# Kernel optimization log

Measured on AMD Instinct MI355X. Metric: run time of the kernel, lower is better.

## Reference

```python
import jax, jax.numpy as jnp
import numpy as np
from jax import lax

B, T, E, D, A, C, FILT = 32, 1600, 1024, 1024, 512, 10, 100
SCALING = 2.0


def setup_inputs() -> dict:
    key = jax.random.key(0)
    ks = jax.random.split(key, 14)
    enc_hs_pad = jax.random.normal(ks[0], (B, T, E), dtype=jnp.float32)
    # lengths in [T//2, T] so every row has valid positions
    enc_hs_len = jax.random.randint(ks[1], (B,), T // 2, T + 1, dtype=jnp.int32)
    dec_z = jax.random.normal(ks[2], (B, D), dtype=jnp.float32)
    # previous attention weights: uniform over valid frames, normalized
    valid = (jnp.arange(T)[None, :] < enc_hs_len[:, None]).astype(jnp.float32)
    raw = jax.random.uniform(ks[3], (B, T), dtype=jnp.float32) * valid
    att_prev = raw / jnp.sum(raw, axis=1, keepdims=True)
    att_h = 0.1 * jax.random.normal(ks[4], (B, A), dtype=jnp.float32)
    att_c = 0.1 * jax.random.normal(ks[5], (B, A), dtype=jnp.float32)
    W_enc = jax.random.normal(ks[6], (A, E), dtype=jnp.float32) / np.sqrt(E)
    b_enc = jax.random.normal(ks[7], (A,), dtype=jnp.float32) * 0.01
    W_dec = jax.random.normal(ks[8], (A, D), dtype=jnp.float32) / np.sqrt(D)
    conv_w = jax.random.normal(ks[9], (C, 1, 2 * FILT + 1), dtype=jnp.float32) / np.sqrt(2 * FILT + 1)
    W_ih = jax.random.normal(ks[10], (4 * A, C), dtype=jnp.float32) / np.sqrt(C)
    W_hh = jax.random.normal(ks[11], (4 * A, A), dtype=jnp.float32) / np.sqrt(A)
    W_g = jax.random.normal(ks[12], (A,), dtype=jnp.float32) / np.sqrt(A)
    b_g = jnp.zeros((1,), dtype=jnp.float32)
    return {"enc_hs_pad": enc_hs_pad, "enc_hs_len": enc_hs_len, "dec_z": dec_z,
            "att_prev": att_prev, "att_h": att_h, "att_c": att_c,
            "W_enc": W_enc, "b_enc": b_enc, "W_dec": W_dec, "conv_w": conv_w,
            "W_ih": W_ih, "W_hh": W_hh, "W_g": W_g, "b_g": b_g}


def reference(enc_hs_pad, enc_hs_len, dec_z, att_prev, att_h, att_c,
              W_enc, b_enc, W_dec, conv_w, W_ih, W_hh, W_g, b_g):
    t_len = enc_hs_pad.shape[1]
    filts = (conv_w.shape[-1] - 1) // 2

    # precompute encoder projection (B, T, A)
    pre_enc = jnp.einsum('bte,ae->bta', enc_hs_pad, W_enc) + b_enc

    # location conv on previous attention: (B,1,T) -> (B,C,T), relu, global max-pool over T
    att_conv = lax.conv_general_dilated(att_prev[:, None, :], conv_w,
                                        window_strides=(1,), padding=[(filts, filts)],
                                        dimension_numbers=('NCH', 'OIH', 'NCH'))
    att_feat = jnp.max(jax.nn.relu(att_conv), axis=-1)  # (B, C)

    # LSTMCell (no bias), pytorch gate order i, f, g, o
    gates = att_feat @ W_ih.T + att_h @ W_hh.T  # (B, 4A)
    i, f, g, o = jnp.split(gates, 4, axis=-1)
    c_new = jax.nn.sigmoid(f) * att_c + jax.nn.sigmoid(i) * jnp.tanh(g)
    h_new = jax.nn.sigmoid(o) * jnp.tanh(c_new)  # (B, A)

    dec_proj = dec_z @ W_dec.T  # (B, A)
    # scores (B, T)
    e = jnp.tanh(h_new[:, None, :] + pre_enc + dec_proj[:, None, :]) @ W_g + b_g

    mask = jnp.arange(t_len)[None, :] >= enc_hs_len[:, None]  # True = pad
    e = jnp.where(mask, jnp.finfo(e.dtype).min, e)
    w = jax.nn.softmax(SCALING * e, axis=1)  # (B, T)

    ctx = jnp.einsum('bt,bte->be', w, enc_hs_pad)  # (B, E)
    return ctx, w, h_new, c_new
```

## Files before the change

kernel.cpp:

```cpp
#include <hip/hip_runtime.h>
#include <hip/hip_bf16.h>

#define BB 32
#define TT 1600
#define EE 1024
#define AA 512
#define CC 10
#define KW 201

typedef __attribute__((ext_vector_type(8))) short short8;
typedef __attribute__((ext_vector_type(4))) float f32x4;

__device__ __forceinline__ float sigm(float x) { return 1.f / (1.f + expf(-x)); }

__device__ __forceinline__ unsigned int cvt2(float a, float b) {
    float2 f2; f2.x = a; f2.y = b;
    __hip_bfloat162 h = __float22bfloat162_rn(f2);
    unsigned int r;
    __builtin_memcpy(&r, &h, 4);
    return r;
}

__device__ __forceinline__ void gl_lds16(const void* g, void* l) {
    __builtin_amdgcn_global_load_lds(
        (const __attribute__((address_space(1))) unsigned int*)g,
        (__attribute__((address_space(3))) unsigned int*)l, 16, 0, 0);
}

#define AF_OFF   0
#define R_OFF    320
#define E_OFF    16704
#define WBF_OFF  67904

#define CTX_OFF 0
#define W_OFF   32768
#define H_OFF   83968
#define C_OFF   100352

__global__ void prep_kernel(const float* __restrict__ att_prev,
                            const float* __restrict__ conv_w,
                            const float* __restrict__ W_enc,
                            float* __restrict__ af,
                            unsigned short* __restrict__ Wbf) {
    int bx = blockIdx.x, tid = threadIdx.x;
    if (bx >= 320) {
        int i = (bx - 320) * 256 + tid;
        float4 v = reinterpret_cast<const float4*>(W_enc)[i];
        uint2 p;
        p.x = cvt2(v.x, v.y);
        p.y = cvt2(v.z, v.w);
        reinterpret_cast<uint2*>(Wbf)[i] = p;
        return;
    }
    int b = bx / 10, c = bx % 10;
    __shared__ float xs[1808];
    __shared__ float wsm[KW];
    __shared__ float red[256];
    const float* xp = att_prev + b * TT;
    for (int i = tid; i < 1808; i += 256) {
        int g = i - 100;
        xs[i] = (g >= 0 && g < TT) ? xp[g] : 0.f;
    }
    if (tid < KW) wsm[tid] = conv_w[c * KW + tid];
    __syncthreads();
    float mx = 0.f;
    #pragma unroll 1
    for (int sweep = 0; sweep < 2; ++sweep) {
        int t0 = sweep * 1024 + tid * 4;
        if (t0 >= TT) break;
        float a0 = xs[t0], a1 = xs[t0 + 1], a2 = xs[t0 + 2], a3 = xs[t0 + 3];
        float s0 = 0.f, s1 = 0.f, s2 = 0.f, s3 = 0.f;
        #pragma unroll 4
        for (int k = 0; k < KW; ++k) {
            float w = wsm[k];
            s0 += w * a0; s1 += w * a1; s2 += w * a2; s3 += w * a3;
            a0 = a1; a1 = a2; a2 = a3;
            a3 = xs[t0 + k + 4];
        }
        mx = fmaxf(mx, fmaxf(fmaxf(s0, s1), fmaxf(s2, s3)));
    }
    red[tid] = mx; __syncthreads();
    for (int s = 128; s > 0; s >>= 1) {
        if (tid < s) red[tid] = fmaxf(red[tid], red[tid + s]);
        __syncthreads();
    }
    if (tid == 0) af[b * CC + c] = red[0];
}

__global__ void gates_lstm_kernel(const float* __restrict__ af,
                                  const float* __restrict__ att_h,
                                  const float* __restrict__ dec_z,
                                  const float* __restrict__ att_c,
                                  const float* __restrict__ W_ih,
                                  const float* __restrict__ W_hh,
                                  const float* __restrict__ W_dec,
                                  float* __restrict__ out,
                                  float* __restrict__ r_ws) {
    __shared__ float gsm[8][32];
    __shared__ float dsm[8][32];
    int tid = threadIdx.x;
    int a0 = blockIdx.x * 2;
    int b = tid & 31;
    if (tid < 256) {
        int u = tid >> 5;
        int gate = u >> 1, ai = u & 1;
        int j = gate * 512 + a0 + ai;
        float s = 0.f;
        #pragma unroll
        for (int k = 0; k < 10; ++k) s += af[b * 10 + k] * W_ih[j * 10 + k];
        const float4* wr = reinterpret_cast<const float4*>(W_hh + (size_t)j * 512);
        const float4* hr = reinterpret_cast<const float4*>(att_h + b * 512);
        #pragma unroll 4
        for (int k = 0; k < 128; ++k) {
            float4 w = wr[k], h = hr[k];
            s += w.x * h.x + w.y * h.y + w.z * h.z + w.w * h.w;
        }
        gsm[u][b] = s;
    } else {
        int v = (tid - 256) >> 5;
        int ai = v & 1, q = v >> 1;
        int a = a0 + ai;
        const float4* wr = reinterpret_cast<const float4*>(W_dec + (size_t)a * 1024) + q * 64;
        const float4* zr = reinterpret_cast<const float4*>(dec_z + (size_t)b * 1024) + q * 64;
        float s = 0.f;
        #pragma unroll 4
        for (int k = 0; k < 64; ++k) {
            float4 w = wr[k], z = zr[k];
            s += w.x * z.x + w.y * z.y + w.z * z.z + w.w * z.w;
        }
        dsm[v][b] = s;
    }
    __syncthreads();
    if (tid < 64) {
        int ai = tid >> 5;
        int a = a0 + ai;
        float ig = gsm[ai][b], fg = gsm[2 + ai][b], gg = gsm[4 + ai][b], og = gsm[6 + ai][b];
        float cn = sigm(fg) * att_c[b * 512 + a] + sigm(ig) * tanhf(gg);
        float hn = sigm(og) * tanhf(cn);
        out[H_OFF + b * 512 + a] = hn;
        out[C_OFF + b * 512 + a] = cn;
        float dec = dsm[ai][b] + dsm[2 + ai][b] + dsm[4 + ai][b] + dsm[6 + ai][b];
        r_ws[b * 512 + a] = hn + dec;
    }
}

__global__ void __launch_bounds__(1024, 4)
score_gemm_kernel(const float* __restrict__ enc,
                  const unsigned short* __restrict__ Wbf,
                  const float* __restrict__ b_enc,
                  const float* __restrict__ r_ws,
                  const float* __restrict__ W_g,
                  float* __restrict__ e_ws) {
    __shared__ __align__(16) short As[2][4096];
    __shared__ __align__(16) short Bs[2][8192];
    __shared__ float e_part[8][128];

    int tid = threadIdx.x;
    int lane = tid & 63, wv = tid >> 6;
    int wm = wv >> 3, wn = wv & 7;
    int col = lane & 15, quad = lane >> 4;
    int m0 = blockIdx.x * 128;

    const unsigned short* bsrc = Wbf + (size_t)((tid >> 6) * 16 + (tid & 15)) * EE
                                 + ((tid >> 4) & 3) * 8;
    int arow = tid >> 3, akq2 = tid & 7;
    const float* asrc = enc + (size_t)(m0 + arow) * EE + akq2 * 4;
    int adst = (arow >> 4) * 512 + ((akq2 >> 1) * 16 + (arow & 15)) * 8 + (akq2 & 1) * 4;

    f32x4 acc[4][2][2];
    #pragma unroll
    for (int mt = 0; mt < 4; ++mt)
        #pragma unroll
        for (int h = 0; h < 2; ++h)
            #pragma unroll
            for (int nt = 0; nt < 2; ++nt)
                acc[mt][h][nt] = (f32x4){0.f, 0.f, 0.f, 0.f};

    {
        gl_lds16(bsrc, &Bs[0][tid * 8]);
        float4 v = *reinterpret_cast<const float4*>(asrc);
        uint2 p; p.x = cvt2(v.x, v.y); p.y = cvt2(v.z, v.w);
        *reinterpret_cast<uint2*>(&As[0][adst]) = p;
    }
    __syncthreads();

    int bufA = 0;
    for (int k0 = 0; k0 < EE; k0 += 32) {
        bool last = (k0 == EE - 32);
        gl_lds16(bsrc + (size_t)256 * EE + k0, &Bs[1][tid * 8]);
        short8 a_frag[4];
        #pragma unroll
        for (int mt = 0; mt < 4; ++mt)
            a_frag[mt] = *reinterpret_cast<const short8*>(
                &As[bufA][(wm * 4 + mt) * 512 + (quad * 16 + col) * 8]);
        #pragma unroll
        for (int nt = 0; nt < 2; ++nt) {
            short8 bf = *reinterpret_cast<const short8*>(
                &Bs[0][(wn * 2 + nt) * 512 + (quad * 16 + col) * 8]);
            #pragma unroll
            for (int mt = 0; mt < 4; ++mt)
                acc[mt][0][nt] = __builtin_amdgcn_mfma_f32_16x16x32_bf16(
                    a_frag[mt], bf, acc[mt][0][nt], 0, 0, 0);
        }
        __syncthreads();
        float4 av;
        if (!last) {
            av = *reinterpret_cast<const float4*>(asrc + k0 + 32);
            gl_lds16(bsrc + k0 + 32, &Bs[0][tid * 8]);
        }
        #pragma unroll
        for (int nt = 0; nt < 2; ++nt) {
            short8 bf = *reinterpret_cast<const short8*>(
                &Bs[1][(wn * 2 + nt) * 512 + (quad * 16 + col) * 8]);
            #pragma unroll
            for (int mt = 0; mt < 4; ++mt)
                acc[mt][1][nt] = __builtin_amdgcn_mfma_f32_16x16x32_bf16(
                    a_frag[mt], bf, acc[mt][1][nt], 0, 0, 0);
        }
        if (!last) {
            uint2 p; p.x = cvt2(av.x, av.y); p.y = cvt2(av.z, av.w);
            *reinterpret_cast<uint2*>(&As[bufA ^ 1][adst]) = p;
        }
        __syncthreads();
        bufA ^= 1;
    }

    float wg[2][2], bn[2][2];
    #pragma unroll
    for (int h = 0; h < 2; ++h)
        #pragma unroll
        for (int nt = 0; nt < 2; ++nt) {
            int n = h * 256 + wn * 32 + nt * 16 + col;
            wg[h][nt] = W_g[n];
            bn[h][nt] = b_enc[n];
        }
    #pragma unroll
    for (int mt = 0; mt < 4; ++mt) {
        int mg = m0 + wm * 64 + mt * 16;
        int bb = mg / TT;
        float rr[2][2];
        #pragma unroll
        for (int h = 0; h < 2; ++h)
            #pragma unroll
            for (int nt = 0; nt < 2; ++nt)
                rr[h][nt] = r_ws[bb * AA + h * 256 + wn * 32 + nt * 16 + col];
        #pragma unroll
        for (int reg = 0; reg < 4; ++reg) {
            float p = 0.f;
            #pragma unroll
            for (int h = 0; h < 2; ++h)
                #pragma unroll
                for (int nt = 0; nt < 2; ++nt)
                    p += wg[h][nt] * tanhf(acc[mt][h][nt][reg] + bn[h][nt] + rr[h][nt]);
            p += __shfl_xor(p, 1);
            p += __shfl_xor(p, 2);
            p += __shfl_xor(p, 4);
            p += __shfl_xor(p, 8);
            if (col == 0) e_part[wn][wm * 64 + mt * 16 + quad * 4 + reg] = p;
        }
    }
    __syncthreads();
    if (tid < 128) {
        float s = 0.f;
        #pragma unroll
        for (int i = 0; i < 8; ++i) s += e_part[i][tid];
        e_ws[m0 + tid] = s;
    }
}

__global__ void ctx_softmax_kernel(const float* __restrict__ enc,
                                   const float* __restrict__ e_ws,
                                   const int* __restrict__ lens,
                                   float* __restrict__ w_out,
                                   float* __restrict__ ctx) {
    int b = blockIdx.x, ch = blockIdx.y;
    int tid = threadIdx.x;
    __shared__ float w_sm[1600];
    __shared__ float red[512];
    __shared__ float part[8][128];
    int len = lens[b];
    const float* e = e_ws + b * TT;
    float mx = -3.4e38f;
    for (int t = tid; t < len; t += 512) mx = fmaxf(mx, e[t]);
    red[tid] = mx; __syncthreads();
    for (int s = 256; s > 0; s >>= 1) {
        if (tid < s) red[tid] = fmaxf(red[tid], red[tid + s]);
        __syncthreads();
    }
    mx = red[0]; __syncthreads();
    float sum = 0.f;
    for (int t = tid; t < TT; t += 512) {
        float p = (t < len) ? expf(2.f * (e[t] - mx)) : 0.f;
        w_sm[t] = p; sum += p;
    }
    red[tid] = sum; __syncthreads();
    for (int s = 256; s > 0; s >>= 1) {
        if (tid < s) red[tid] += red[tid + s];
        __syncthreads();
    }
    float inv = 1.f / red[0];
    __syncthreads();
    for (int t = tid; t < TT; t += 512) {
        float wv = w_sm[t] * inv;
        w_sm[t] = wv;
        if (ch == 0) w_out[b * TT + t] = wv;
    }
    __syncthreads();
    int lane2 = tid & 63, w8 = tid >> 6;
    int tb = w8 * 200;
    const float* base = enc + (size_t)(b * TT + tb) * EE + ch * 128 + lane2 * 2;
    float cx = 0.f, cy = 0.f;
    #pragma unroll 1
    for (int i = 0; i < 200; i += 8) {
        #pragma unroll
        for (int j = 0; j < 8; ++j) {
            float2 v = *reinterpret_cast<const float2*>(base + (size_t)(i + j) * EE);
            float ww = w_sm[tb + i + j];
            cx += ww * v.x; cy += ww * v.y;
        }
    }
    part[w8][lane2 * 2] = cx;
    part[w8][lane2 * 2 + 1] = cy;
    __syncthreads();
    if (tid < 128) {
        float s = 0.f;
        #pragma unroll
        for (int i = 0; i < 8; ++i) s += part[i][tid];
        ctx[b * EE + ch * 128 + tid] = s;
    }
}

extern "C" void kernel_launch(void* const* d_in, const int* in_sizes, int n_in,
                              void* d_out, int out_size, void* d_ws, size_t ws_size,
                              hipStream_t stream) {
    const float* enc      = (const float*)d_in[0];
    const int*   lens     = (const int*)d_in[1];
    const float* dec_z    = (const float*)d_in[2];
    const float* att_prev = (const float*)d_in[3];
    const float* att_h    = (const float*)d_in[4];
    const float* att_c    = (const float*)d_in[5];
    const float* W_enc    = (const float*)d_in[6];
    const float* b_enc    = (const float*)d_in[7];
    const float* W_dec    = (const float*)d_in[8];
    const float* conv_w   = (const float*)d_in[9];
    const float* W_ih     = (const float*)d_in[10];
    const float* W_hh     = (const float*)d_in[11];
    const float* W_g      = (const float*)d_in[12];

    float* out = (float*)d_out;
    float* ws  = (float*)d_ws;
    float* af   = ws + AF_OFF;
    float* r_ws = ws + R_OFF;
    float* e_ws = ws + E_OFF;
    unsigned short* Wbf = (unsigned short*)(ws + WBF_OFF);

    prep_kernel<<<832, 256, 0, stream>>>(att_prev, conv_w, W_enc, af, Wbf);
    gates_lstm_kernel<<<256, 512, 0, stream>>>(af, att_h, dec_z, att_c,
                                               W_ih, W_hh, W_dec, out, r_ws);
    score_gemm_kernel<<<400, 1024, 0, stream>>>(enc, Wbf, b_enc, r_ws, W_g, e_ws);
    ctx_softmax_kernel<<<dim3(BB, 8), 512, 0, stream>>>(enc, e_ws, lens,
                                                        out + W_OFF, out + CTX_OFF);
}
```

Measured before the change: 497.1 us.

## Retile score GEMM to 64-row blocks and split softmax and context kernels

After: 532.4 us. 7.1% more time.

```diff
diff --git a/kernel.cpp b/kernel.cpp
--- a/kernel.cpp
+++ b/kernel.cpp
@@ -41,8 +41,14 @@
                             const float* __restrict__ conv_w,
                             const float* __restrict__ W_enc,
                             float* __restrict__ af,
-                            unsigned short* __restrict__ Wbf) {
+                            unsigned short* __restrict__ Wbf,
+                            float* __restrict__ out) {
     int bx = blockIdx.x, tid = threadIdx.x;
+    if (bx >= 832) {
+        int i = (bx - 832) * 256 + tid;
+        reinterpret_cast<float4*>(out + CTX_OFF)[i] = (float4){0.f, 0.f, 0.f, 0.f};
+        return;
+    }
     if (bx >= 320) {
         int i = (bx - 320) * 256 + tid;
         float4 v = reinterpret_cast<const float4*>(W_enc)[i];
@@ -144,123 +150,102 @@
     }
 }
 
-__global__ void __launch_bounds__(1024, 4)
+__global__ void __launch_bounds__(512, 2)
 score_gemm_kernel(const float* __restrict__ enc,
                   const unsigned short* __restrict__ Wbf,
                   const float* __restrict__ b_enc,
                   const float* __restrict__ r_ws,
                   const float* __restrict__ W_g,
                   float* __restrict__ e_ws) {
-    __shared__ __align__(16) short As[2][4096];
-    __shared__ __align__(16) short Bs[2][8192];
-    __shared__ float e_part[8][128];
+    __shared__ __align__(16) float As[512 * 4];
+    __shared__ __align__(16) short Bs[2048 * 8];
+    __shared__ float e_part[8][64];
 
     int tid = threadIdx.x;
     int lane = tid & 63, wv = tid >> 6;
-    int wm = wv >> 3, wn = wv & 7;
     int col = lane & 15, quad = lane >> 4;
-    int m0 = blockIdx.x * 128;
-
-    const unsigned short* bsrc = Wbf + (size_t)((tid >> 6) * 16 + (tid & 15)) * EE
-                                 + ((tid >> 4) & 3) * 8;
-    int arow = tid >> 3, akq2 = tid & 7;
-    const float* asrc = enc + (size_t)(m0 + arow) * EE + akq2 * 4;
-    int adst = (arow >> 4) * 512 + ((akq2 >> 1) * 16 + (arow & 15)) * 8 + (akq2 & 1) * 4;
-
-    f32x4 acc[4][2][2];
+    int m0 = blockIdx.x * 64;
+
+    {
+    }
+    int a_row = tid >> 3;
+    int a_kg = (tid & 7) ^ (a_row & 7);
+    const float* a_src = enc + (size_t)(m0 + a_row) * EE + a_kg * 4;
+    const unsigned short* b_src[4];
+    #pragma unroll
+    for (int j = 0; j < 4; ++j) {
+        int s = tid + 512 * j;
+        int n = s >> 2;
+        int kg = (s & 3) ^ ((n >> 1) & 3);
+        b_src[j] = Wbf + (size_t)n * EE + kg * 8;
+    }
+
+    f32x4 acc[4][4];
     #pragma unroll
     for (int mt = 0; mt < 4; ++mt)
         #pragma unroll
-        for (int h = 0; h < 2; ++h)
-            #pragma unroll
-            for (int nt = 0; nt < 2; ++nt)
-                acc[mt][h][nt] = (f32x4){0.f, 0.f, 0.f, 0.f};
-
-    {
-        gl_lds16(bsrc, &Bs[0][tid * 8]);
-        float4 v = *reinterpret_cast<const float4*>(asrc);
-        uint2 p; p.x = cvt2(v.x, v.y); p.y = cvt2(v.z, v.w);
-        *reinterpret_cast<uint2*>(&As[0][adst]) = p;
-    }
-    __syncthreads();
-
-    int bufA = 0;
+        for (int nt = 0; nt < 4; ++nt)
+            acc[mt][nt] = (f32x4){0.f, 0.f, 0.f, 0.f};
+
+    int aswz = col & 7;
+    int bswz = (col >> 1) & 3;
+
     for (int k0 = 0; k0 < EE; k0 += 32) {
-        bool last = (k0 == EE - 32);
-        gl_lds16(bsrc + (size_t)256 * EE + k0, &Bs[1][tid * 8]);
+        __syncthreads();
+        gl_lds16(a_src + k0, &As[tid * 4]);
+        #pragma unroll
+        for (int j = 0; j < 4; ++j)
+            gl_lds16(b_src[j] + k0, &Bs[(tid + 512 * j) * 8]);
+        __syncthreads();
+
         short8 a_frag[4];
         #pragma unroll
-        for (int mt = 0; mt < 4; ++mt)
-            a_frag[mt] = *reinterpret_cast<const short8*>(
-                &As[bufA][(wm * 4 + mt) * 512 + (quad * 16 + col) * 8]);
-        #pragma unroll
-        for (int nt = 0; nt < 2; ++nt) {
-            short8 bf = *reinterpret_cast<const short8*>(
-                &Bs[0][(wn * 2 + nt) * 512 + (quad * 16 + col) * 8]);
+        for (int mt = 0; mt < 4; ++mt) {
+            int s0 = (mt * 16 + col) * 8 + ((2 * quad) ^ aswz);
+            float4 fa = *reinterpret_cast<const float4*>(&As[s0 * 4]);
+            float4 fb = *reinterpret_cast<const float4*>(&As[(s0 ^ 1) * 4]);
+            uint4 u;
+            u.x = cvt2(fa.x, fa.y); u.y = cvt2(fa.z, fa.w);
+            u.z = cvt2(fb.x, fb.y); u.w = cvt2(fb.z, fb.w);
+            __builtin_memcpy(&a_frag[mt], &u, 16);
+        }
+        #pragma unroll
+        for (int nt = 0; nt < 4; ++nt) {
+            int slot = (wv * 64 + nt * 16 + col) * 4 + (quad ^ bswz);
+            short8 bf = *reinterpret_cast<const short8*>(&Bs[slot * 8]);
             #pragma unroll
             for (int mt = 0; mt < 4; ++mt)
-                acc[mt][0][nt] = __builtin_amdgcn_mfma_f32_16x16x32_bf16(
-                    a_frag[mt], bf, acc[mt][0][nt], 0, 0, 0);
-        }
-        __syncthreads();
-        float4 av;
-        if (!last) {
-            av = *reinterpret_cast<const float4*>(asrc + k0 + 32);
-            gl_lds16(bsrc + k0 + 32, &Bs[0][tid * 8]);
-        }
-        #pragma unroll
-        for (int nt = 0; nt < 2; ++nt) {
-            short8 bf = *reinterpret_cast<const short8*>(
-                &Bs[1][(wn * 2 + nt) * 512 + (quad * 16 + col) * 8]);
-            #pragma unroll
-            for (int mt = 0; mt < 4; ++mt)
-                acc[mt][1][nt] = __builtin_amdgcn_mfma_f32_16x16x32_bf16(
-                    a_frag[mt], bf, acc[mt][1][nt], 0, 0, 0);
-        }
-        if (!last) {
-            uint2 p; p.x = cvt2(av.x, av.y); p.y = cvt2(av.z, av.w);
-            *reinterpret_cast<uint2*>(&As[bufA ^ 1][adst]) = p;
-        }
-        __syncthreads();
-        bufA ^= 1;
-    }
-
-    float wg[2][2], bn[2][2];
+                acc[mt][nt] = __builtin_amdgcn_mfma_f32_16x16x32_bf16(
+                    a_frag[mt], bf, acc[mt][nt], 0, 0, 0);
+        }
+    }
+
+    int bb = blockIdx.x / 25;
+    float wg[4], bn[4], rr[4];
     #pragma unroll
-    for (int h = 0; h < 2; ++h)
-        #pragma unroll
-        for (int nt = 0; nt < 2; ++nt) {
-            int n = h * 256 + wn * 32 + nt * 16 + col;
-            wg[h][nt] = W_g[n];
-            bn[h][nt] = b_enc[n];
-        }
+    for (int nt = 0; nt < 4; ++nt) {
+        int n = wv * 64 + nt * 16 + col;
+        wg[nt] = W_g[n];
+        bn[nt] = b_enc[n];
+        rr[nt] = r_ws[bb * AA + n];
+    }
     #pragma unroll
     for (int mt = 0; mt < 4; ++mt) {
-        int mg = m0 + wm * 64 + mt * 16;
-        int bb = mg / TT;
-        float rr[2][2];
-        #pragma unroll
-        for (int h = 0; h < 2; ++h)
-            #pragma unroll
-            for (int nt = 0; nt < 2; ++nt)
-                rr[h][nt] = r_ws[bb * AA + h * 256 + wn * 32 + nt * 16 + col];
         #pragma unroll
         for (int reg = 0; reg < 4; ++reg) {
             float p = 0.f;
             #pragma unroll
-            for (int h = 0; h < 2; ++h)
-                #pragma unroll
-                for (int nt = 0; nt < 2; ++nt)
-                    p += wg[h][nt] * tanhf(acc[mt][h][nt][reg] + bn[h][nt] + rr[h][nt]);
+            for (int nt = 0; nt < 4; ++nt)
+                p += wg[nt] * tanhf(acc[mt][nt][reg] + bn[nt] + rr[nt]);
             p += __shfl_xor(p, 1);
             p += __shfl_xor(p, 2);
             p += __shfl_xor(p, 4);
             p += __shfl_xor(p, 8);
-            if (col == 0) e_part[wn][wm * 64 + mt * 16 + quad * 4 + reg] = p;
+            if (col == 0) e_part[wv][mt * 16 + quad * 4 + reg] = p;
         }
     }
     __syncthreads();
-    if (tid < 128) {
+    if (tid < 64) {
         float s = 0.f;
         #pragma unroll
         for (int i = 0; i < 8; ++i) s += e_part[i][tid];
@@ -268,66 +253,58 @@
     }
 }
 
-__global__ void ctx_softmax_kernel(const float* __restrict__ enc,
-                                   const float* __restrict__ e_ws,
-                                   const int* __restrict__ lens,
-                                   float* __restrict__ w_out,
-                                   float* __restrict__ ctx) {
-    int b = blockIdx.x, ch = blockIdx.y;
-    int tid = threadIdx.x;
-    __shared__ float w_sm[1600];
-    __shared__ float red[512];
-    __shared__ float part[8][128];
+__global__ void softmax_kernel(const float* __restrict__ e_ws,
+                               const int* __restrict__ lens,
+                               float* __restrict__ w_out) {
+    int b = blockIdx.x, tid = threadIdx.x;
     int len = lens[b];
     const float* e = e_ws + b * TT;
+    __shared__ float red[256];
     float mx = -3.4e38f;
-    for (int t = tid; t < len; t += 512) mx = fmaxf(mx, e[t]);
+    for (int t = tid; t < len; t += 256) mx = fmaxf(mx, e[t]);
     red[tid] = mx; __syncthreads();
-    for (int s = 256; s > 0; s >>= 1) {
+    for (int s = 128; s > 0; s >>= 1) {
         if (tid < s) red[tid] = fmaxf(red[tid], red[tid + s]);
         __syncthreads();
     }
     mx = red[0]; __syncthreads();
     float sum = 0.f;
-    for (int t = tid; t < TT; t += 512) {
-        float p = (t < len) ? expf(2.f * (e[t] - mx)) : 0.f;
-        w_sm[t] = p; sum += p;
-    }
+    for (int t = tid; t < len; t += 256) sum += expf(2.f * (e[t] - mx));
     red[tid] = sum; __syncthreads();
-    for (int s = 256; s > 0; s >>= 1) {
+    for (int s = 128; s > 0; s >>= 1) {
         if (tid < s) red[tid] += red[tid + s];
         __syncthreads();
     }
     float inv = 1.f / red[0];
-    __syncthreads();
-    for (int t = tid; t < TT; t += 512) {
-        float wv = w_sm[t] * inv;
-        w_sm[t] = wv;
-        if (ch == 0) w_out[b * TT + t] = wv;
-    }
-    __syncthreads();
-    int lane2 = tid & 63, w8 = tid >> 6;
-    int tb = w8 * 200;
-    const float* base = enc + (size_t)(b * TT + tb) * EE + ch * 128 + lane2 * 2;
-    float cx = 0.f, cy = 0.f;
+    for (int t = tid; t < TT; t += 256)
+        w_out[b * TT + t] = (t < len) ? expf(2.f * (e[t] - mx)) * inv : 0.f;
+}
+
+__global__ void ctx_kernel(const float* __restrict__ enc,
+                           const float* __restrict__ w,
+                           float* __restrict__ ctx) {
+    int b = blockIdx.x, seg = blockIdx.y;
+    int t0 = seg * 64;
+    const float* wrow = w + b * TT + t0;
+    const float* base = enc + ((size_t)(b * TT + t0)) * EE + threadIdx.x * 4;
+    float4 acc = {0.f, 0.f, 0.f, 0.f};
     #pragma unroll 1
-    for (int i = 0; i < 200; i += 8) {
-        #pragma unroll
-        for (int j = 0; j < 8; ++j) {
-            float2 v = *reinterpret_cast<const float2*>(base + (size_t)(i + j) * EE);
-            float ww = w_sm[tb + i + j];
-            cx += ww * v.x; cy += ww * v.y;
-        }
-    }
-    part[w8][lane2 * 2] = cx;
-    part[w8][lane2 * 2 + 1] = cy;
-    __syncthreads();
-    if (tid < 128) {
-        float s = 0.f;
-        #pragma unroll
-        for (int i = 0; i < 8; ++i) s += part[i][tid];
-        ctx[b * EE + ch * 128 + tid] = s;
-    }
+    for (int i = 0; i < 64; i += 4) {
+        float w0 = wrow[i], w1 = wrow[i + 1], w2 = wrow[i + 2], w3 = wrow[i + 3];
+        float4 v0 = *reinterpret_cast<const float4*>(base + (size_t)(i + 0) * EE);
+        float4 v1 = *reinterpret_cast<const float4*>(base + (size_t)(i + 1) * EE);
+        float4 v2 = *reinterpret_cast<const float4*>(base + (size_t)(i + 2) * EE);
+        float4 v3 = *reinterpret_cast<const float4*>(base + (size_t)(i + 3) * EE);
+        acc.x += w0 * v0.x + w1 * v1.x + w2 * v2.x + w3 * v3.x;
+        acc.y += w0 * v0.y + w1 * v1.y + w2 * v2.y + w3 * v3.y;
+        acc.z += w0 * v0.z + w1 * v1.z + w2 * v2.z + w3 * v3.z;
+        acc.w += w0 * v0.w + w1 * v1.w + w2 * v2.w + w3 * v3.w;
+    }
+    float* dst = ctx + b * EE + threadIdx.x * 4;
+    atomicAdd(dst + 0, acc.x);
+    atomicAdd(dst + 1, acc.y);
+    atomicAdd(dst + 2, acc.z);
+    atomicAdd(dst + 3, acc.w);
 }
 
 extern "C" void kernel_launch(void* const* d_in, const int* in_sizes, int n_in,
@@ -354,10 +331,10 @@
     float* e_ws = ws + E_OFF;
     unsigned short* Wbf = (unsigned short*)(ws + WBF_OFF);
 
-    prep_kernel<<<832, 256, 0, stream>>>(att_prev, conv_w, W_enc, af, Wbf);
+    prep_kernel<<<864, 256, 0, stream>>>(att_prev, conv_w, W_enc, af, Wbf, out);
     gates_lstm_kernel<<<256, 512, 0, stream>>>(af, att_h, dec_z, att_c,
                                                W_ih, W_hh, W_dec, out, r_ws);
-    score_gemm_kernel<<<400, 1024, 0, stream>>>(enc, Wbf, b_enc, r_ws, W_g, e_ws);
-    ctx_softmax_kernel<<<dim3(BB, 8), 512, 0, stream>>>(enc, e_ws, lens,
-                                                        out + W_OFF, out + CTX_OFF);
-}
+    score_gemm_kernel<<<800, 512, 0, stream>>>(enc, Wbf, b_enc, r_ws, W_g, e_ws);
+    softmax_kernel<<<BB, 256, 0, stream>>>(e_ws, lens, out + W_OFF);
+    ctx_kernel<<<dim3(BB, 25), 256, 0, stream>>>(enc, out + W_OFF, out + CTX_OFF);
+}
```
